# Optimization experiments

Measured on AMD Instinct MI355X. Metric: run time of the kernel, lower is better.

## Reference

```python
import jax, jax.numpy as jnp
import numpy as np

N, E, B, F_IN, C, K = 200000, 3200000, 128, 128, 10, 30
D_CAT = 97  # 32+32+32+1 concatenated GCN outputs


def setup_inputs() -> dict:
    key = jax.random.key(0)
    ks = jax.random.split(key, 12)
    s = 0.1
    return {
        "x": jax.random.normal(ks[0], (N, F_IN), jnp.float32),
        "edge_index": jax.random.randint(ks[1], (2, E), 0, N, jnp.int32),
        "batch": jnp.sort(jax.random.randint(ks[2], (N,), 0, B, jnp.int32)),
        "W1": jax.random.normal(ks[3], (F_IN, 32), jnp.float32) * s,
        "b1": jnp.zeros((32,), jnp.float32),
        "W2": jax.random.normal(ks[4], (32, 32), jnp.float32) * s,
        "b2": jnp.zeros((32,), jnp.float32),
        "W3": jax.random.normal(ks[5], (32, 32), jnp.float32) * s,
        "b3": jnp.zeros((32,), jnp.float32),
        "W4": jax.random.normal(ks[6], (32, 1), jnp.float32) * s,
        "b4": jnp.zeros((1,), jnp.float32),
        "conv5_w": jax.random.normal(ks[7], (16, 1, 97), jnp.float32) * s,
        "conv5_b": jnp.zeros((16,), jnp.float32),
        "conv6_w": jax.random.normal(ks[8], (32, 16, 5), jnp.float32) * s,
        "conv6_b": jnp.zeros((32,), jnp.float32),
        "fc1_w": jax.random.normal(ks[9], (352, 128), jnp.float32) * s,
        "fc1_b": jnp.zeros((128,), jnp.float32),
        "fc2_w": jax.random.normal(ks[10], (128, C), jnp.float32) * s,
        "fc2_b": jnp.zeros((C,), jnp.float32),
    }


def _gcn(x, W, b, src, dst, enorm, self_norm):
    # PyG GCNConv: h = xW; out = sum_j norm_ij * h_j (incl. self loop) + b
    h = x @ W
    agg = jax.ops.segment_sum(h[src] * enorm[:, None], dst, num_segments=h.shape[0])
    return agg + h * self_norm[:, None] + b


def _conv1d(x, w, b, stride):
    y = jax.lax.conv_general_dilated(x, w, (stride,), 'VALID',
                                     dimension_numbers=('NCH', 'OIH', 'NCH'))
    return y + b[None, :, None]


def reference(x, edge_index, batch, W1, b1, W2, b2, W3, b3, W4, b4,
              conv5_w, conv5_b, conv6_w, conv6_b, fc1_w, fc1_b, fc2_w, fc2_b):
    src, dst = edge_index[0], edge_index[1]
    # remove_self_loops (zero edge weight) then GCN adds self loop of weight 1
    w = (src != dst).astype(x.dtype)
    deg = jax.ops.segment_sum(w, dst, num_segments=N) + 1.0
    dinv = jax.lax.rsqrt(deg)
    enorm = w * dinv[src] * dinv[dst]   # per-edge sym norm
    self_norm = 1.0 / deg               # self-loop norm = dinv[i]^2

    x1 = jnp.tanh(_gcn(x, W1, b1, src, dst, enorm, self_norm))
    x2 = jnp.tanh(_gcn(x1, W2, b2, src, dst, enorm, self_norm))
    x3 = jnp.tanh(_gcn(x2, W3, b3, src, dst, enorm, self_norm))
    x4 = jnp.tanh(_gcn(x3, W4, b4, src, dst, enorm, self_norm))
    xc = jnp.concatenate([x1, x2, x3, x4], axis=-1)  # [N, 97]

    # SortAggregation(k=30): per-graph top-k nodes by last channel (descending)
    keyf = xc[:, -1]
    graph_ids = jnp.arange(B, dtype=batch.dtype)
    scores = jnp.where(batch[None, :] == graph_ids[:, None], keyf[None, :],
                       jnp.float32(-jnp.inf))         # [B, N]
    topv, topi = jax.lax.top_k(scores, K)              # [B, K]
    feats = xc[topi]                                   # [B, K, 97]
    feats = jnp.where(jnp.isfinite(topv)[..., None], feats, 0.0)  # pad rows -> 0
    z = feats.reshape(B, 1, K * D_CAT)                 # [B, 1, 2910]

    z = jax.nn.relu(_conv1d(z, conv5_w, conv5_b, 97))  # [B, 16, 30]
    z = jax.lax.reduce_window(z, -jnp.inf, jax.lax.max,
                              (1, 1, 2), (1, 1, 2), 'VALID')  # [B, 16, 15]
    z = jax.nn.relu(_conv1d(z, conv6_w, conv6_b, 1))   # [B, 32, 11]
    z = z.reshape(B, -1)                               # [B, 352]
    h = jax.nn.relu(z @ fc1_w + fc1_b)                 # dropout = identity (eval)
    return jax.nn.log_softmax(h @ fc2_w + fc2_b, axis=-1)
```

## Files before the change

### kernel.cpp

```cpp
#include <hip/hip_runtime.h>
#include <math.h>

#define TPB 256
#define TOPK 30
#define NGRAPH 128
#define TKCAP 4096
#define BSHIFT 11
#define NBMAX 128
#define FSHIFT 8
#define NFMAX 800
#define FCAP 4608


__global__ void bhist(const int* __restrict__ src, const int* __restrict__ dst,
                      int* __restrict__ btot, int E) {
    __shared__ int bcnt[NBMAX];
    int t = threadIdx.x;
    int base = blockIdx.x * 2048;
    int lim = E - base; if (lim > 2048) lim = 2048;
    for (int i = t; i < NBMAX; i += 256) bcnt[i] = 0;
    __syncthreads();
    for (int i = t; i < lim; i += 256) {
        int s = src[base + i], d = dst[base + i];
        if (s != d) atomicAdd(&bcnt[d >> BSHIFT], 1);
    }
    __syncthreads();
    for (int i = t; i < NBMAX; i += 256)
        if (bcnt[i] > 0) atomicAdd(&btot[i], bcnt[i]);
}

__global__ void bucket_scan(const int* __restrict__ btot, int* __restrict__ bbase,
                            int nbuckets) {
    __shared__ int ls[NBMAX];
    int t = threadIdx.x;
    int v = (t < nbuckets) ? btot[t] : 0;
    ls[t] = v;
    __syncthreads();
    for (int o = 1; o < NBMAX; o <<= 1) {
        int x = 0;
        if (t >= o) x = ls[t - o];
        __syncthreads();
        ls[t] += x;
        __syncthreads();
    }
    if (t < nbuckets) bbase[t] = ls[t] - v;
}

__global__ void bin_edges(const int* __restrict__ src, const int* __restrict__ dst,
                          const int* __restrict__ bbase_g, int* __restrict__ gcur,
                          int2* __restrict__ scratch, int E) {
    __shared__ int2 eds[2048];
    __shared__ int bcnt[NBMAX], bbase[NBMAX], boff[NBMAX];
    int t = threadIdx.x;
    int base = blockIdx.x * 2048;
    int lim = E - base; if (lim > 2048) lim = 2048;
    for (int i = t; i < NBMAX; i += 256) { bcnt[i] = 0; boff[i] = 0; }
    __syncthreads();
    for (int i = t; i < lim; i += 256) {
        int s = src[base + i], d = dst[base + i];
        if (s == d) d = -1;
        eds[i] = make_int2(s, d);
        if (d >= 0) atomicAdd(&bcnt[d >> BSHIFT], 1);
    }
    __syncthreads();
    for (int i = t; i < NBMAX; i += 256) {
        if (bcnt[i] > 0)
            bbase[i] = bbase_g[i] + atomicAdd(&gcur[i], bcnt[i]);
    }
    __syncthreads();
    for (int i = t; i < lim; i += 256) {
        int2 ed = eds[i];
        if (ed.y >= 0) {
            int b = ed.y >> BSHIFT;
            int pos = bbase[b] + atomicAdd(&boff[b], 1);
            scratch[pos] = ed;
        }
    }
}

__global__ void bucket_count(const int2* __restrict__ scratch,
                             const int* __restrict__ bbase, const int* __restrict__ btot,
                             int* __restrict__ rowptr, float* __restrict__ dinv,
                             float* __restrict__ snorm, int N, int NB) {
    __shared__ int hist[1 << BSHIFT];
    __shared__ int ls2[256];
    int b = blockIdx.x, t = threadIdx.x;
    int nlo = b << BSHIFT;
    int nn = N - nlo; if (nn > (1 << BSHIFT)) nn = 1 << BSHIFT;
    for (int i = t; i < (1 << BSHIFT); i += 256) hist[i] = 0;
    __syncthreads();
    int lo = bbase[b], hi = lo + btot[b];
    for (int e = lo + t; e < hi; e += 256)
        atomicAdd(&hist[scratch[e].y - nlo], 1);
    __syncthreads();
    int loc[8]; int run = 0;
    #pragma unroll
    for (int j = 0; j < 8; ++j) { loc[j] = run; run += hist[t * 8 + j]; }
    ls2[t] = run;
    __syncthreads();
    for (int o = 1; o < 256; o <<= 1) {
        int x = (t >= o) ? ls2[t - o] : 0;
        __syncthreads();
        ls2[t] += x;
        __syncthreads();
    }
    int base = bbase[b] + ls2[t] - run;
    #pragma unroll
    for (int j = 0; j < 8; ++j) {
        int i = t * 8 + j;
        if (i < nn) {
            rowptr[nlo + i] = base + loc[j];
            int c = hist[i];
            float deg = (float)c + 1.0f;
            dinv[nlo + i] = 1.0f / sqrtf(deg);
            snorm[nlo + i] = 1.0f / deg;
        }
    }
    if (b == NB - 1 && t == 0) rowptr[N] = bbase[b] + btot[b];
}

__global__ void bin2(const int2* __restrict__ scratch, const int* __restrict__ rowptr,
                     int* __restrict__ fcur, int2* __restrict__ scratch2, int N, int E) {
    __shared__ int fcnt[NFMAX], fbase[NFMAX], foff[NFMAX];
    int t = threadIdx.x;
    int En = rowptr[N];
    int base = blockIdx.x * 8192;
    if (base >= En) return;
    int lim = En - base; if (lim > 8192) lim = 8192;
    for (int i = t; i < NFMAX; i += 256) { fcnt[i] = 0; foff[i] = 0; }
    __syncthreads();
    for (int i = t; i < lim; i += 256) {
        int d = scratch[base + i].y;
        atomicAdd(&fcnt[d >> FSHIFT], 1);
    }
    __syncthreads();
    for (int fi = t; fi < NFMAX; fi += 256) {
        if (fcnt[fi] > 0)
            fbase[fi] = rowptr[fi << FSHIFT] + atomicAdd(&fcur[fi], fcnt[fi]);
    }
    __syncthreads();
    for (int i = t; i < lim; i += 256) {
        int2 ed = scratch[base + i];
        int fi = ed.y >> FSHIFT;
        int pos = fbase[fi] + atomicAdd(&foff[fi], 1);
        scratch2[pos] = ed;
    }
}

__global__ __launch_bounds__(256) void scatter_sort(const int2* __restrict__ scratch2,
                                                    const int* __restrict__ rowptr,
                                                    const float* __restrict__ dinv,
                                                    int2* __restrict__ eprec, int N) {
    __shared__ int srcA[FCAP], dstA[FCAP], inv[FCAP];
    __shared__ int hist[1 << FSHIFT];
    __shared__ int hcur[1 << FSHIFT];
    int f = blockIdx.x, t = threadIdx.x;
    int nlo = f << FSHIFT;
    int nhi = nlo + (1 << FSHIFT); if (nhi > N) nhi = N;
    int lo = rowptr[nlo], hi = rowptr[nhi];
    int span = hi - lo;
    for (int i = t; i < (1 << FSHIFT); i += 256) hist[i] = 0;
    __syncthreads();
    if (span <= FCAP) {
        for (int i = t; i < span; i += 256) {
            int2 ed = scratch2[lo + i];
            srcA[i] = ed.x; dstA[i] = ed.y;
            atomicAdd(&hist[ed.y - nlo], 1);
        }
        __syncthreads();
        int v = hist[t];
        hcur[t] = v;
        __syncthreads();
        for (int o = 1; o < 256; o <<= 1) {
            int x = (t >= o) ? hcur[t - o] : 0;
            __syncthreads();
            hcur[t] += x;
            __syncthreads();
        }
        int excl = hcur[t] - v;
        __syncthreads();
        hcur[t] = excl;
        __syncthreads();
        for (int i = t; i < span; i += 256) {
            int slot = atomicAdd(&hcur[dstA[i] - nlo], 1);
            inv[slot] = i;
        }
        __syncthreads();
        for (int p = t; p < span; p += 256) {
            int i = inv[p];
            int s = srcA[i], d = dstA[i];
            eprec[lo + p] = make_int2(s, __float_as_int(dinv[s] * dinv[d]));
        }
    } else {
        for (int e = lo + t; e < hi; e += 256) {
            int2 ed = scratch2[e];
            int d = ed.y;
            int p = rowptr[d] + atomicAdd(&hist[d - nlo], 1);
            eprec[p] = make_int2(ed.x, __float_as_int(dinv[ed.x] * dinv[d]));
        }
    }
}


__global__ void mm_128_32(const float* __restrict__ X, const float* __restrict__ W,
                          float* __restrict__ H, int n) {
    __shared__ float Ws[128 * 32];
    __shared__ float xs[32 * 128];
    int t = threadIdx.x;
    int rbase = blockIdx.x * 32;
    #pragma unroll
    for (int j = 0; j < 4; ++j) {
        int idx = t + 256 * j;
        *(float4*)(Ws + idx * 4) = *(const float4*)(W + idx * 4);
        int row = rbase + (idx >> 5);
        float4 v = make_float4(0.f, 0.f, 0.f, 0.f);
        if (row < n) v = *(const float4*)(X + (long)rbase * 128 + idx * 4);
        *(float4*)(xs + idx * 4) = v;
    }
    __syncthreads();
    int c4 = (t & 7) * 4, r = t >> 3;
    int row = rbase + r;
    if (row >= n) return;
    float ac0 = 0.f, ac1 = 0.f, ac2 = 0.f, ac3 = 0.f;
    #pragma unroll 8
    for (int k0 = 0; k0 < 128; k0 += 4) {
        float4 xv = *(const float4*)(xs + r * 128 + k0);
        #pragma unroll
        for (int j = 0; j < 4; ++j) {
            float xj = (j == 0) ? xv.x : (j == 1) ? xv.y : (j == 2) ? xv.z : xv.w;
            float4 wv = *(const float4*)(Ws + (k0 + j) * 32 + c4);
            ac0 += xj * wv.x; ac1 += xj * wv.y; ac2 += xj * wv.z; ac3 += xj * wv.w;
        }
    }
    *(float4*)(H + (long)row * 32 + c4) = make_float4(ac0, ac1, ac2, ac3);
}

__global__ void mm_32_32(const float* __restrict__ X, const float* __restrict__ W,
                         float* __restrict__ H, int n) {
    __shared__ float Ws[32 * 32];
    __shared__ float xs[32 * 32];
    int t = threadIdx.x;
    int rbase = blockIdx.x * 32;
    {
        *(float4*)(Ws + t * 4) = *(const float4*)(W + t * 4);
        int row = rbase + (t >> 3);
        float4 v = make_float4(0.f, 0.f, 0.f, 0.f);
        if (row < n) v = *(const float4*)(X + (long)rbase * 32 + t * 4);
        *(float4*)(xs + t * 4) = v;
    }
    __syncthreads();
    int c4 = (t & 7) * 4, r = t >> 3;
    int row = rbase + r;
    if (row >= n) return;
    float ac0 = 0.f, ac1 = 0.f, ac2 = 0.f, ac3 = 0.f;
    #pragma unroll
    for (int k0 = 0; k0 < 32; k0 += 4) {
        float4 xv = *(const float4*)(xs + r * 32 + k0);
        #pragma unroll
        for (int j = 0; j < 4; ++j) {
            float xj = (j == 0) ? xv.x : (j == 1) ? xv.y : (j == 2) ? xv.z : xv.w;
            float4 wv = *(const float4*)(Ws + (k0 + j) * 32 + c4);
            ac0 += xj * wv.x; ac1 += xj * wv.y; ac2 += xj * wv.z; ac3 += xj * wv.w;
        }
    }
    *(float4*)(H + (long)row * 32 + c4) = make_float4(ac0, ac1, ac2, ac3);
}

__global__ void mm_32_1(const float* __restrict__ X, const float* __restrict__ W,
                        float* __restrict__ H4, int n) {
    int gid = blockIdx.x * blockDim.x + threadIdx.x;
    int node = gid >> 3, l = gid & 7;
    if (node >= n) return;
    float4 v = *(const float4*)(X + (long)node * 32 + l * 4);
    float s = v.x * W[l * 4] + v.y * W[l * 4 + 1] + v.z * W[l * 4 + 2] + v.w * W[l * 4 + 3];
    s += __shfl_xor(s, 1, 64);
    s += __shfl_xor(s, 2, 64);
    s += __shfl_xor(s, 4, 64);
    if (l == 0) H4[node] = s;
}


__global__ void agg32(const float* __restrict__ H, const int2* __restrict__ eprec,
                      const int* __restrict__ rowptr,
                      const float* __restrict__ snorm, const float* __restrict__ bias,
                      float* __restrict__ OUT, int n) {
    int gid = blockIdx.x * blockDim.x + threadIdx.x;
    int node = gid >> 3, l = gid & 7;
    if (node >= n) return;
    int beg = rowptr[node], end = rowptr[node + 1];
    float ax = 0.f, ay = 0.f, az = 0.f, aw = 0.f;
    int e0 = beg;
    for (; e0 + 8 <= end; e0 += 8) {
        int2 ed = eprec[e0 + l];
        int ss[8]; float ww[8];
        #pragma unroll
        for (int j = 0; j < 8; ++j) {
            ss[j] = __shfl(ed.x, j, 8);
            ww[j] = __shfl(__int_as_float(ed.y), j, 8);
        }
        float4 hv[8];
        #pragma unroll
        for (int j = 0; j < 8; ++j)
            hv[j] = *(const float4*)(H + (long)ss[j] * 32 + l * 4);
        #pragma unroll
        for (int j = 0; j < 8; ++j) {
            ax += hv[j].x * ww[j]; ay += hv[j].y * ww[j];
            az += hv[j].z * ww[j]; aw += hv[j].w * ww[j];
        }
    }
    if (e0 < end) {
        int m = end - e0;
        int2 ed = (l < m) ? eprec[e0 + l] : make_int2(0, 0);
        for (int j = 0; j < m; ++j) {
            int s = __shfl(ed.x, j, 8);
            float w = __shfl(__int_as_float(ed.y), j, 8);
            float4 hv = *(const float4*)(H + (long)s * 32 + l * 4);
            ax += hv.x * w; ay += hv.y * w; az += hv.z * w; aw += hv.w * w;
        }
    }
    float sn = snorm[node];
    float4 hv = *(const float4*)(H + (long)node * 32 + l * 4);
    float4 bv = *(const float4*)(bias + l * 4);
    float4 o;
    o.x = tanhf(ax + hv.x * sn + bv.x);
    o.y = tanhf(ay + hv.y * sn + bv.y);
    o.z = tanhf(az + hv.z * sn + bv.z);
    o.w = tanhf(aw + hv.w * sn + bv.w);
    *(float4*)(OUT + (long)node * 32 + l * 4) = o;
}

__global__ void agg1(const float* __restrict__ H4, const int2* __restrict__ eprec,
                     const int* __restrict__ rowptr,
                     const float* __restrict__ snorm, const float* __restrict__ b4,
                     float* __restrict__ X4, int n) {
    int node = blockIdx.x * blockDim.x + threadIdx.x;
    if (node >= n) return;
    int beg = rowptr[node], end = rowptr[node + 1];
    float acc = 0.f;
    for (int e = beg; e < end; ++e) {
        int2 ed = eprec[e];
        acc += H4[ed.x] * __int_as_float(ed.y);
    }
    X4[node] = tanhf(acc + H4[node] * snorm[node] + b4[0]);
}


__global__ void graph_start(const int* __restrict__ batch, int* __restrict__ gstart,
                            int n, int B) {
    int i = blockIdx.x * blockDim.x + threadIdx.x;
    if (i >= n) return;
    int b = batch[i];
    int bp = (i == 0) ? -1 : batch[i - 1];
    for (int g = bp + 1; g <= b; ++g) gstart[g] = i;
    if (i == n - 1) {
        for (int g = b + 1; g <= B; ++g) gstart[g] = n;
    }
}


__global__ __launch_bounds__(256) void topk_head(
        const float* __restrict__ x1, const float* __restrict__ x2,
        const float* __restrict__ x3, const float* __restrict__ x4,
        const int* __restrict__ gstart,
        const float* __restrict__ w5, const float* __restrict__ b5,
        const float* __restrict__ w6, const float* __restrict__ b6,
        const float* __restrict__ fw1, const float* __restrict__ fb1,
        const float* __restrict__ fw2, const float* __restrict__ fb2,
        float* __restrict__ out) {
    int g = blockIdx.x;
    int t = threadIdx.x;
    __shared__ int topi_l[TOPK];
    __shared__ int selg[TOPK];
    __shared__ float lv[4 * TOPK];
    __shared__ int li[4 * TOPK];
    __shared__ float vals[TKCAP];
    __shared__ float wbv[4];
    __shared__ int wbi[4];
    __shared__ float feats[TOPK][97];
    __shared__ float c5[16][30];
    __shared__ float p6[16][15];
    __shared__ float z[352];
    __shared__ float hh[128];
    __shared__ float oo[10];

    int beg = gstart[g], end = gstart[g + 1];
    int range = end - beg;

    if (range <= 2048) {
        int wv = t >> 6, l = t & 63;
        int chunk = (range + 3) >> 2;
        int cbeg = wv * chunk;
        int cend = cbeg + chunk; if (cend > range) cend = range;
        float rv[8];
        #pragma unroll
        for (int j = 0; j < 8; ++j) {
            int i = cbeg + l + (j << 6);
            rv[j] = (i < cend) ? x4[beg + i] : -INFINITY;
        }
        for (int k = 0; k < TOPK; ++k) {
            float best = -INFINITY;
            int bj = -1;
            #pragma unroll
            for (int j = 0; j < 8; ++j)
                if (rv[j] > best) { best = rv[j]; bj = j; }
            int bi = (bj < 0) ? 0x7fffffff : cbeg + (bj << 6) + l;
            #pragma unroll
            for (int off = 1; off < 64; off <<= 1) {
                float ov = __shfl_xor(best, off, 64);
                int oi = __shfl_xor(bi, off, 64);
                if (ov > best || (ov == best && oi < bi)) { best = ov; bi = oi; }
            }
            if (l == 0) { lv[wv * TOPK + k] = best; li[wv * TOPK + k] = bi; }
            if (bi != 0x7fffffff && ((bi - cbeg) & 63) == l) {
                int wj = (bi - cbeg) >> 6;
                #pragma unroll
                for (int j = 0; j < 8; ++j)
                    if (j == wj) rv[j] = -INFINITY;
            }
        }
        __syncthreads();
        if (t < 64) {
            float mv0 = lv[t];
            int   mi0 = li[t];
            int i1 = t + 64;
            float mv1 = (i1 < 120) ? lv[i1] : -INFINITY;
            int   mi1 = (i1 < 120) ? li[i1] : 0x7fffffff;
            for (int k = 0; k < TOPK; ++k) {
                float best = mv0; int bi = mi0;
                if (mv1 > best || (mv1 == best && mi1 < bi)) { best = mv1; bi = mi1; }
                #pragma unroll
                for (int off = 1; off < 64; off <<= 1) {
                    float ov = __shfl_xor(best, off, 64);
                    int oi = __shfl_xor(bi, off, 64);
                    if (ov > best || (ov == best && oi < bi)) { best = ov; bi = oi; }
                }
                if (t == 0)
                    topi_l[k] = (bi == 0x7fffffff) ? -1 : beg + bi;
                if (mi0 == bi) mv0 = -INFINITY;
                if (mi1 == bi) mv1 = -INFINITY;
            }
        }
    } else {
        int lim = range < TKCAP ? range : TKCAP;
        for (int i = t; i < lim; i += 256) vals[i] = x4[beg + i];
        __syncthreads();
        for (int k = 0; k < TOPK; ++k) {
            float best = -INFINITY;
            int bi = 0x7fffffff;
            for (int i = t; i < lim; i += 256) {
                float v = vals[i];
                if (v > best) { best = v; bi = i; }
            }
            for (int i = TKCAP + t; i < range; i += 256) {
                int gi = beg + i;
                bool taken = false;
                for (int j = 0; j < k; ++j)
                    if (selg[j] == gi) { taken = true; break; }
                if (taken) continue;
                float v = x4[gi];
                if (v > best || (v == best && i < bi)) { best = v; bi = i; }
            }
            #pragma unroll
            for (int off = 1; off < 64; off <<= 1) {
                float ov = __shfl_xor(best, off, 64);
                int oi = __shfl_xor(bi, off, 64);
                if (ov > best || (ov == best && oi < bi)) { best = ov; bi = oi; }
            }
            if ((t & 63) == 0) { wbv[t >> 6] = best; wbi[t >> 6] = bi; }
            __syncthreads();
            if (t == 0) {
                float bv = wbv[0]; int bi0 = wbi[0];
                for (int wq = 1; wq < 4; ++wq)
                    if (wbv[wq] > bv || (wbv[wq] == bv && wbi[wq] < bi0)) { bv = wbv[wq]; bi0 = wbi[wq]; }
                int gl = (bi0 == 0x7fffffff) ? -1 : beg + bi0;
                selg[k] = gl;
                topi_l[k] = gl;
                if (bi0 != 0x7fffffff && bi0 < TKCAP) vals[bi0] = -INFINITY;
            }
            __syncthreads();
        }
    }
    __syncthreads();

    for (int idx = t; idx < TOPK * 97; idx += 256) {
        int k = idx / 97, j = idx % 97;
        int node = topi_l[k];
        float v = 0.f;
        if (node >= 0) {
            if (j < 32) v = x1[(long)node * 32 + j];
            else if (j < 64) v = x2[(long)node * 32 + (j - 32)];
            else if (j < 96) v = x3[(long)node * 32 + (j - 64)];
            else v = x4[node];
        }
        feats[k][j] = v;
    }
    __syncthreads();

    for (int idx = t; idx < 16 * 30; idx += 256) {
        int oc = idx / 30, k = idx % 30;
        float acc = b5[oc];
        for (int j = 0; j < 97; ++j) acc += w5[oc * 97 + j] * feats[k][j];
        c5[oc][k] = fmaxf(acc, 0.f);
    }
    __syncthreads();

    for (int idx = t; idx < 16 * 15; idx += 256) {
        int oc = idx / 15, k = idx % 15;
        p6[oc][k] = fmaxf(c5[oc][2 * k], c5[oc][2 * k + 1]);
    }
    __syncthreads();

    for (int idx = t; idx < 32 * 11; idx += 256) {
        int oc = idx / 11, tt = idx % 11;
        float acc = b6[oc];
        for (int ic = 0; ic < 16; ++ic)
            for (int j = 0; j < 5; ++j)
                acc += w6[(oc * 16 + ic) * 5 + j] * p6[ic][tt + j];
        z[idx] = fmaxf(acc, 0.f);
    }
    __syncthreads();

    if (t < 128) {
        float acc = fb1[t];
        for (int i = 0; i < 352; ++i) acc += z[i] * fw1[i * 128 + t];
        hh[t] = fmaxf(acc, 0.f);
    }
    __syncthreads();

    if (t < 10) {
        float acc = fb2[t];
        for (int j = 0; j < 128; ++j) acc += hh[j] * fw2[j * 10 + t];
        oo[t] = acc;
    }
    __syncthreads();

    if (t < 10) {
        float m = -INFINITY;
        for (int c = 0; c < 10; ++c) m = fmaxf(m, oo[c]);
        float s = 0.f;
        for (int c = 0; c < 10; ++c) s += expf(oo[c] - m);
        out[g * 10 + t] = oo[t] - m - logf(s);
    }
}


extern "C" void kernel_launch(void* const* d_in, const int* in_sizes, int n_in,
                              void* d_out, int out_size, void* d_ws, size_t ws_size,
                              hipStream_t stream) {
    const float* x     = (const float*)d_in[0];
    const int*   ei    = (const int*)d_in[1];
    const int*   batch = (const int*)d_in[2];
    const float* W1 = (const float*)d_in[3];
    const float* b1 = (const float*)d_in[4];
    const float* W2 = (const float*)d_in[5];
    const float* b2 = (const float*)d_in[6];
    const float* W3 = (const float*)d_in[7];
    const float* b3 = (const float*)d_in[8];
    const float* W4 = (const float*)d_in[9];
    const float* b4 = (const float*)d_in[10];
    const float* w5 = (const float*)d_in[11];
    const float* b5 = (const float*)d_in[12];
    const float* w6 = (const float*)d_in[13];
    const float* b6 = (const float*)d_in[14];
    const float* fw1 = (const float*)d_in[15];
    const float* fb1 = (const float*)d_in[16];
    const float* fw2 = (const float*)d_in[17];
    const float* fb2 = (const float*)d_in[18];

    const int N = in_sizes[0] / 128;
    const int E = in_sizes[1] / 2;
    const int* src = ei;
    const int* dst = ei + E;

    char* w = (char*)d_ws;
    size_t off = 0;
    auto alloc = [&](size_t bytes) -> void* {
        void* p = w + off;
        off = (off + bytes + 255) & ~(size_t)255;
        return p;
    };

    int*   gcur   = (int*)alloc(NBMAX * 4);
    int*   btot   = (int*)alloc(NBMAX * 4);
    int*   fcur   = (int*)alloc(NFMAX * 4);
    int*   bbase  = (int*)alloc(NBMAX * 4);
    int*   gstart = (int*)alloc((size_t)(NGRAPH + 1) * 4);
    int*   rowptr = (int*)alloc((size_t)(N + 1) * 4);
    float* dinv   = (float*)alloc((size_t)N * 4);
    float* snorm  = (float*)alloc((size_t)N * 4);
    int2*  eprec  = (int2*)alloc((size_t)E * 8);
    float* hbuf   = (float*)alloc((size_t)N * 32 * 4);
    float* x1     = (float*)alloc((size_t)N * 32 * 4);
    float* x2     = (float*)alloc((size_t)N * 32 * 4);
    float* x3     = (float*)alloc((size_t)N * 32 * 4);
    float* h4     = (float*)alloc((size_t)N * 4);
    float* x4     = (float*)alloc((size_t)N * 4);

    int2* scratch  = (int2*)hbuf;
    int2* scratch2 = (int2*)x1;

    hipMemsetAsync(gcur, 0, (size_t)(2 * NBMAX + NFMAX) * 4, stream);

    const int NB = (N + (1 << BSHIFT) - 1) >> BSHIFT;
    const int NF = (N + (1 << FSHIFT) - 1) >> FSHIFT;
    const int EB = (E + 2047) / 2048;

    graph_start<<<(N + TPB - 1) / TPB, TPB, 0, stream>>>(batch, gstart, N, NGRAPH);
    bhist<<<EB, TPB, 0, stream>>>(src, dst, btot, E);
    bucket_scan<<<1, NBMAX, 0, stream>>>(btot, bbase, NB);
    bin_edges<<<EB, TPB, 0, stream>>>(src, dst, bbase, gcur, scratch, E);
    bucket_count<<<NB, TPB, 0, stream>>>(scratch, bbase, btot, rowptr, dinv, snorm, N, NB);
    bin2<<<(E + 8191) / 8192, TPB, 0, stream>>>(scratch, rowptr, fcur, scratch2, N, E);
    scatter_sort<<<NF, 256, 0, stream>>>(scratch2, rowptr, dinv, eprec, N);

    mm_128_32<<<(N + 31) / 32, 256, 0, stream>>>(x, W1, hbuf, N);
    agg32<<<((size_t)N * 8 + TPB - 1) / TPB, TPB, 0, stream>>>(hbuf, eprec, rowptr,
                                                               snorm, b1, x1, N);
    mm_32_32<<<(N + 31) / 32, 256, 0, stream>>>(x1, W2, hbuf, N);
    agg32<<<((size_t)N * 8 + TPB - 1) / TPB, TPB, 0, stream>>>(hbuf, eprec, rowptr,
                                                               snorm, b2, x2, N);
    mm_32_32<<<(N + 31) / 32, 256, 0, stream>>>(x2, W3, hbuf, N);
    agg32<<<((size_t)N * 8 + TPB - 1) / TPB, TPB, 0, stream>>>(hbuf, eprec, rowptr,
                                                               snorm, b3, x3, N);
    mm_32_1<<<((size_t)N * 8 + TPB - 1) / TPB, TPB, 0, stream>>>(x3, W4, h4, N);
    agg1<<<(N + TPB - 1) / TPB, TPB, 0, stream>>>(h4, eprec, rowptr, snorm, b4, x4, N);

    topk_head<<<NGRAPH, 256, 0, stream>>>(x1, x2, x3, x4, gstart,
                                          w5, b5, w6, b6, fw1, fb1, fw2, fb2,
                                          (float*)d_out);
}
```

Measured before the change: 568.8 us.

## Widen topk_head to 512 threads, prefetch head weights into LDS during top-k

Doubles topk_head's block size. The extra four waves copy the conv5, conv6 and fc2 weights into shared memory while the original waves run the per-graph top-k selection. The fc1 reduction is split across four partial sums before a final combine. The intent is to hide global weight latency behind the selection and shorten the serial head, at the cost of more shared memory per block and a larger launch.

```diff
diff --git a/kernel.cpp b/kernel.cpp
--- a/kernel.cpp
+++ b/kernel.cpp
@@ -358,7 +358,7 @@
 }
 
 
-__global__ __launch_bounds__(256) void topk_head(
+__global__ __launch_bounds__(512) void topk_head(
         const float* __restrict__ x1, const float* __restrict__ x2,
         const float* __restrict__ x3, const float* __restrict__ x4,
         const int* __restrict__ gstart,
@@ -374,8 +374,12 @@
     __shared__ float lv[4 * TOPK];
     __shared__ int li[4 * TOPK];
     __shared__ float vals[TKCAP];
-    __shared__ float wbv[4];
-    __shared__ int wbi[4];
+    __shared__ float wbv[8];
+    __shared__ int wbi[8];
+    __shared__ float ws5[16 * 97];
+    __shared__ float ws6[32 * 16 * 5];
+    __shared__ float wf2[128 * 10];
+    __shared__ float part[4][128];
     __shared__ float feats[TOPK][97];
     __shared__ float c5[16][30];
     __shared__ float p6[16][15];
@@ -387,35 +391,42 @@
     int range = end - beg;
 
     if (range <= 2048) {
-        int wv = t >> 6, l = t & 63;
-        int chunk = (range + 3) >> 2;
-        int cbeg = wv * chunk;
-        int cend = cbeg + chunk; if (cend > range) cend = range;
-        float rv[8];
-        #pragma unroll
-        for (int j = 0; j < 8; ++j) {
-            int i = cbeg + l + (j << 6);
-            rv[j] = (i < cend) ? x4[beg + i] : -INFINITY;
-        }
-        for (int k = 0; k < TOPK; ++k) {
-            float best = -INFINITY;
-            int bj = -1;
+        if (t >= 256) {
+            int u = t - 256;
+            for (int i = u; i < 16 * 97; i += 256) ws5[i] = w5[i];
+            for (int i = u; i < 32 * 16 * 5; i += 256) ws6[i] = w6[i];
+            for (int i = u; i < 128 * 10; i += 256) wf2[i] = fw2[i];
+        } else {
+            int wv = t >> 6, l = t & 63;
+            int chunk = (range + 3) >> 2;
+            int cbeg = wv * chunk;
+            int cend = cbeg + chunk; if (cend > range) cend = range;
+            float rv[8];
             #pragma unroll
-            for (int j = 0; j < 8; ++j)
-                if (rv[j] > best) { best = rv[j]; bj = j; }
-            int bi = (bj < 0) ? 0x7fffffff : cbeg + (bj << 6) + l;
-            #pragma unroll
-            for (int off = 1; off < 64; off <<= 1) {
-                float ov = __shfl_xor(best, off, 64);
-                int oi = __shfl_xor(bi, off, 64);
-                if (ov > best || (ov == best && oi < bi)) { best = ov; bi = oi; }
+            for (int j = 0; j < 8; ++j) {
+                int i = cbeg + l + (j << 6);
+                rv[j] = (i < cend) ? x4[beg + i] : -INFINITY;
             }
-            if (l == 0) { lv[wv * TOPK + k] = best; li[wv * TOPK + k] = bi; }
-            if (bi != 0x7fffffff && ((bi - cbeg) & 63) == l) {
-                int wj = (bi - cbeg) >> 6;
+            for (int k = 0; k < TOPK; ++k) {
+                float best = -INFINITY;
+                int bj = -1;
                 #pragma unroll
                 for (int j = 0; j < 8; ++j)
-                    if (j == wj) rv[j] = -INFINITY;
+                    if (rv[j] > best) { best = rv[j]; bj = j; }
+                int bi = (bj < 0) ? 0x7fffffff : cbeg + (bj << 6) + l;
+                #pragma unroll
+                for (int off = 1; off < 64; off <<= 1) {
+                    float ov = __shfl_xor(best, off, 64);
+                    int oi = __shfl_xor(bi, off, 64);
+                    if (ov > best || (ov == best && oi < bi)) { best = ov; bi = oi; }
+                }
+                if (l == 0) { lv[wv * TOPK + k] = best; li[wv * TOPK + k] = bi; }
+                if (bi != 0x7fffffff && ((bi - cbeg) & 63) == l) {
+                    int wj = (bi - cbeg) >> 6;
+                    #pragma unroll
+                    for (int j = 0; j < 8; ++j)
+                        if (j == wj) rv[j] = -INFINITY;
+                }
             }
         }
         __syncthreads();
@@ -441,17 +452,23 @@
             }
         }
     } else {
+        if (t >= 256) {
+            int u = t - 256;
+            for (int i = u; i < 16 * 97; i += 256) ws5[i] = w5[i];
+            for (int i = u; i < 32 * 16 * 5; i += 256) ws6[i] = w6[i];
+            for (int i = u; i < 128 * 10; i += 256) wf2[i] = fw2[i];
+        }
         int lim = range < TKCAP ? range : TKCAP;
-        for (int i = t; i < lim; i += 256) vals[i] = x4[beg + i];
+        for (int i = t; i < lim; i += 512) vals[i] = x4[beg + i];
         __syncthreads();
         for (int k = 0; k < TOPK; ++k) {
             float best = -INFINITY;
             int bi = 0x7fffffff;
-            for (int i = t; i < lim; i += 256) {
+            for (int i = t; i < lim; i += 512) {
                 float v = vals[i];
                 if (v > best) { best = v; bi = i; }
             }
-            for (int i = TKCAP + t; i < range; i += 256) {
+            for (int i = TKCAP + t; i < range; i += 512) {
                 int gi = beg + i;
                 bool taken = false;
                 for (int j = 0; j < k; ++j)
@@ -470,7 +487,7 @@
             __syncthreads();
             if (t == 0) {
                 float bv = wbv[0]; int bi0 = wbi[0];
-                for (int wq = 1; wq < 4; ++wq)
+                for (int wq = 1; wq < 8; ++wq)
                     if (wbv[wq] > bv || (wbv[wq] == bv && wbi[wq] < bi0)) { bv = wbv[wq]; bi0 = wbi[wq]; }
                 int gl = (bi0 == 0x7fffffff) ? -1 : beg + bi0;
                 selg[k] = gl;
@@ -482,7 +499,7 @@
     }
     __syncthreads();
 
-    for (int idx = t; idx < TOPK * 97; idx += 256) {
+    for (int idx = t; idx < TOPK * 97; idx += 512) {
         int k = idx / 97, j = idx % 97;
         int node = topi_l[k];
         float v = 0.f;
@@ -496,40 +513,47 @@
     }
     __syncthreads();
 
-    for (int idx = t; idx < 16 * 30; idx += 256) {
+    for (int idx = t; idx < 16 * 30; idx += 512) {
         int oc = idx / 30, k = idx % 30;
         float acc = b5[oc];
-        for (int j = 0; j < 97; ++j) acc += w5[oc * 97 + j] * feats[k][j];
+        for (int j = 0; j < 97; ++j) acc += ws5[oc * 97 + j] * feats[k][j];
         c5[oc][k] = fmaxf(acc, 0.f);
     }
     __syncthreads();
 
-    for (int idx = t; idx < 16 * 15; idx += 256) {
+    for (int idx = t; idx < 16 * 15; idx += 512) {
         int oc = idx / 15, k = idx % 15;
         p6[oc][k] = fmaxf(c5[oc][2 * k], c5[oc][2 * k + 1]);
     }
     __syncthreads();
 
-    for (int idx = t; idx < 32 * 11; idx += 256) {
+    for (int idx = t; idx < 32 * 11; idx += 512) {
         int oc = idx / 11, tt = idx % 11;
         float acc = b6[oc];
         for (int ic = 0; ic < 16; ++ic)
             for (int j = 0; j < 5; ++j)
-                acc += w6[(oc * 16 + ic) * 5 + j] * p6[ic][tt + j];
+                acc += ws6[(oc * 16 + ic) * 5 + j] * p6[ic][tt + j];
         z[idx] = fmaxf(acc, 0.f);
     }
     __syncthreads();
 
+    {
+        int o = t & 127, s = t >> 7;
+        float acc = 0.f;
+        int i0 = s * 88, i1 = i0 + 88;
+        for (int i = i0; i < i1; ++i) acc += z[i] * fw1[i * 128 + o];
+        part[s][o] = acc;
+    }
+    __syncthreads();
     if (t < 128) {
-        float acc = fb1[t];
-        for (int i = 0; i < 352; ++i) acc += z[i] * fw1[i * 128 + t];
-        hh[t] = fmaxf(acc, 0.f);
+        float v = fb1[t] + ((part[0][t] + part[1][t]) + (part[2][t] + part[3][t]));
+        hh[t] = fmaxf(v, 0.f);
     }
     __syncthreads();
 
     if (t < 10) {
         float acc = fb2[t];
-        for (int j = 0; j < 128; ++j) acc += hh[j] * fw2[j * 10 + t];
+        for (int j = 0; j < 128; ++j) acc += hh[j] * wf2[j * 10 + t];
         oo[t] = acc;
     }
     __syncthreads();
@@ -625,7 +649,7 @@
     mm_32_1<<<((size_t)N * 8 + TPB - 1) / TPB, TPB, 0, stream>>>(x3, W4, h4, N);
     agg1<<<(N + TPB - 1) / TPB, TPB, 0, stream>>>(h4, eprec, rowptr, snorm, b4, x4, N);
 
-    topk_head<<<NGRAPH, 256, 0, stream>>>(x1, x2, x3, x4, gstart,
+    topk_head<<<NGRAPH, 512, 0, stream>>>(x1, x2, x3, x4, gstart,
                                           w5, b5, w6, b6, fw1, fb1, fw2, fb2,
                                           (float*)d_out);
 }
```

New measurement: 554.5 us. -2.5%, faster.
